# Kernel optimization log

Hardware: AMD Instinct MI355X
Metric: run time of the kernel (lower is better)

The kernel has to match this reference:

```python
import jax, jax.numpy as jnp
import numpy as np

P_SIZE = 5
NUM_HEAD = 8
GN_EPS = 1e-5


def _conv1x1(w, x, b=None):
    # w: (out_c, in_c), x: (n, in_c, h, w)
    y = jnp.einsum('oc,nchw->nohw', w, x)
    if b is not None:
        y = y + b[None, :, None, None]
    return y


def _leaky_relu(x, slope=0.2):
    return jnp.where(x >= 0, x, slope * x)


def _bilinear_sample_zeros(feat, vx, vy):
    # feat: (c, H, W); vx, vy: (p2, H, W) pixel coords (align_corners=True,
    # padding_mode='zeros'). Returns (c, p2, H, W).
    c, H, W = feat.shape
    x0 = jnp.floor(vx)
    y0 = jnp.floor(vy)
    x1 = x0 + 1.0
    y1 = y0 + 1.0
    wx1 = vx - x0
    wy1 = vy - y0
    wx0 = 1.0 - wx1
    wy0 = 1.0 - wy1

    def corner(xi, yi, wgt):
        valid = (xi >= 0) & (xi <= W - 1) & (yi >= 0) & (yi <= H - 1)
        xc = jnp.clip(xi, 0, W - 1).astype(jnp.int32)
        yc = jnp.clip(yi, 0, H - 1).astype(jnp.int32)
        g = feat[:, yc, xc]  # (c, p2, H, W)
        return g * (wgt * valid)[None]

    return (corner(x0, y0, wx0 * wy0) + corner(x1, y0, wx1 * wy0)
            + corner(x0, y1, wx0 * wy1) + corner(x1, y1, wx1 * wy1))


def _deform_coords(deform_field, h, w, p_size):
    # deform_field: (n, 2, h, w) -> vx, vy: (n, p2, h, w) pixel coords.
    pad = (p_size - 1) // 2
    gy, gx = jnp.meshgrid(jnp.arange(h, dtype=deform_field.dtype),
                          jnp.arange(w, dtype=deform_field.dtype), indexing='ij')
    shift = jnp.arange(p_size, dtype=deform_field.dtype) - pad
    sy, sx = jnp.meshgrid(shift, shift, indexing='ij')
    sy = sy.reshape(-1, 1, 1)
    sx = sx.reshape(-1, 1, 1)
    vx = gx[None] + sx + deform_field[:, None, 0]  # (n, p2, h, w)
    vy = gy[None] + sy + deform_field[:, None, 1]
    return vx, vy


def _transformer_forward(query, key, value, deform_field,
                         w_q, w_k, w_v, w_fc,
                         mlp_w1, mlp_b1, mlp_w2, mlp_b2, gn_w, gn_b):
    p2 = P_SIZE * P_SIZE
    q = _conv1x1(w_q, query)
    k = _conv1x1(w_k, key)
    v = _conv1x1(w_v, value)
    n, c, h, w = q.shape
    d_k = c // NUM_HEAD

    vx, vy = _deform_coords(deform_field, h, w, P_SIZE)
    sample = jax.vmap(_bilinear_sample_zeros)  # over batch
    k_s = sample(k, vx, vy)  # (n, c, p2, h, w)
    v_s = sample(v, vx, vy)

    qh = q.reshape(n, NUM_HEAD, d_k, h, w)
    kh = k_s.reshape(n, NUM_HEAD, d_k, p2, h, w)
    vh = v_s.reshape(n, NUM_HEAD, d_k, p2, h, w)

    scale = 1.0 / jnp.sqrt(jnp.asarray(d_k, q.dtype))
    scores = jnp.einsum('nedyx,nedpyx->neyxp', qh * scale, kh)
    attn = jax.nn.softmax(scores, axis=-1)
    out = jnp.einsum('neyxp,nedpyx->nedyx', attn, vh).reshape(n, c, h, w)
    out = _conv1x1(w_fc, out)

    hid = _leaky_relu(_conv1x1(mlp_w1, out, mlp_b1))
    out = out + _conv1x1(mlp_w2, hid, mlp_b2)

    # GroupNorm(1, c): normalize over (c, h, w) per sample
    mean = jnp.mean(out, axis=(1, 2, 3), keepdims=True)
    var = jnp.var(out, axis=(1, 2, 3), keepdims=True)
    out = (out - mean) * jax.lax.rsqrt(var + GN_EPS)
    out = out * gn_w[None, :, None, None] + gn_b[None, :, None, None]
    return out


def setup_inputs() -> dict:
    key = jax.random.key(0)
    ks = jax.random.split(key, 12)
    n, C, H, W = 1, 128, 128, 128
    hidden = C * 2
    s = 1.0 / np.sqrt(C)
    return {
        'query': jax.random.normal(ks[0], (n, C, H, W), jnp.float32),
        'key': jax.random.normal(ks[1], (n, C, H, W), jnp.float32),
        'value': jax.random.normal(ks[2], (n, C, H, W), jnp.float32),
        'deform_field': jax.random.normal(ks[3], (n, 2, H, W), jnp.float32) * 2.0,
        'w_q': jax.random.normal(ks[4], (C, C), jnp.float32) * s,
        'w_k': jax.random.normal(ks[5], (C, C), jnp.float32) * s,
        'w_v': jax.random.normal(ks[6], (C, C), jnp.float32) * s,
        'w_fc': jax.random.normal(ks[7], (C, C), jnp.float32) * s,
        'mlp_w1': jax.random.normal(ks[8], (hidden, C), jnp.float32) * s,
        'mlp_b1': jnp.zeros((hidden,), jnp.float32),
        'mlp_w2': jax.random.normal(ks[9], (C, hidden), jnp.float32) * (1.0 / np.sqrt(hidden)),
        'mlp_b2': jnp.zeros((C,), jnp.float32),
        'gn_w': jnp.ones((C,), jnp.float32),
        'gn_b': jnp.zeros((C,), jnp.float32),
    }


def reference(query, key, value, deform_field, w_q, w_k, w_v, w_fc,
              mlp_w1, mlp_b1, mlp_w2, mlp_b2, gn_w, gn_b):
    return _transformer_forward(query, key, value, deform_field,
                                w_q, w_k, w_v, w_fc,
                                mlp_w1, mlp_b1, mlp_w2, mlp_b2, gn_w, gn_b)
```

## Files before the change

kernel.cpp:

```cpp
#include <hip/hip_runtime.h>
#include <hip/hip_bf16.h>

#define HW 16384
#define W 128
#define C 128
#define HID 256

typedef __attribute__((ext_vector_type(8))) short short8v;
typedef __attribute__((ext_vector_type(4))) float f32x4;

__device__ __forceinline__ unsigned short f2bf(float f) {
    union { float f; unsigned u; } x; x.f = f;
    unsigned r = x.u + 0x7FFF + ((x.u >> 16) & 1);
    return (unsigned short)(r >> 16);
}
__device__ __forceinline__ float bf2f(unsigned short b) {
    union { unsigned u; float f; } x; x.u = ((unsigned)b) << 16;
    return x.f;
}

__device__ __forceinline__ void stage_load(const unsigned short* __restrict__ src,
                                           short8v* r, int t) {
    #pragma unroll
    for (int c = 0; c < 8; ++c)
        r[c] = *(const short8v*)(src + (size_t)(c * 256 + t) * 8);
}
template<int RSH>
__device__ __forceinline__ void stage_write(const short8v* r, unsigned short* lds, int t) {
    #pragma unroll
    for (int c = 0; c < 8; ++c) {
        int gi = c * 256 + t;
        int row = gi >> RSH, colg = gi & ((1 << RSH) - 1);
        *(short8v*)(lds + (size_t)(((row << RSH) + (colg ^ (row & 7))) << 3)) = r[c];
    }
}
template<int RSH>
__device__ __forceinline__ void stage32(const unsigned short* __restrict__ src,
                                        unsigned short* lds, int t) {
    #pragma unroll
    for (int c = 0; c < 8; ++c) {
        int gi = c * 256 + t;
        int row = gi >> RSH, colg = gi & ((1 << RSH) - 1);
        short8v v = *(const short8v*)(src + (size_t)gi * 8);
        *(short8v*)(lds + (size_t)(((row << RSH) + (colg ^ (row & 7))) << 3)) = v;
    }
}

__global__ void prep_weights(const float* __restrict__ wq, const float* __restrict__ wk,
                             const float* __restrict__ wv, const float* __restrict__ wfc,
                             const float* __restrict__ w1, const float* __restrict__ w2,
                             unsigned short* __restrict__ wb) {
    int i = blockIdx.x * 256 + threadIdx.x;
    float v;
    if (i < 16384)       v = wq[i];
    else if (i < 32768)  v = wk[i - 16384];
    else if (i < 49152)  v = wv[i - 32768];
    else if (i < 65536)  v = wfc[i - 49152];
    else if (i < 98304)  v = w1[i - 65536];
    else                 v = w2[i - 98304];
    wb[i] = f2bf(v);
}

__global__ __launch_bounds__(256, 2)
void qkv_mfma(const float* __restrict__ q_in, const float* __restrict__ k_in,
              const float* __restrict__ v_in, const unsigned short* __restrict__ wb,
              unsigned short* __restrict__ q_t, unsigned short* __restrict__ kv_t) {
    __shared__ unsigned short lx[3][32 * 128];
    __shared__ unsigned short wbuf[16384];
    const int t = threadIdx.x;
    const int p0 = blockIdx.x * 32;
    const int lane = t & 63, row16 = lane & 15, g = lane >> 4;
    const int w = t >> 6, nh = w & 1, mh = w >> 1;
    const int ploc = nh * 16 + row16;
    const int pix = p0 + ploc;
    const int swz = (ploc & 7) << 3;

    stage32<4>(wb, wbuf, t);

    const float* ins[3] = {q_in, k_in, v_in};
    #pragma unroll
    for (int m = 0; m < 3; ++m) {
        #pragma unroll
        for (int it = 0; it < 16; ++it) {
            int e = t + 256 * it;
            int p = e & 31, c = e >> 5;
            lx[m][p * 128 + (c ^ ((p & 7) << 3))] = f2bf(ins[m][c * HW + p0 + p]);
        }
    }

    #pragma unroll 1
    for (int m = 0; m < 3; ++m) {
        if (m > 0) {
            __syncthreads();
            stage32<4>(wb + m * 16384, wbuf, t);
        }
        __syncthreads();

        f32x4 acc[4] = {};
        #pragma unroll
        for (int kk = 0; kk < 4; ++kk) {
            short8v b = *(const short8v*)&lx[m][ploc * 128 + ((kk * 32 + g * 8) ^ swz)];
            #pragma unroll
            for (int f = 0; f < 4; ++f) {
                int row = mh * 64 + f * 16 + row16;
                short8v a = *(const short8v*)&wbuf[(row << 7) + (((kk * 4 + g) ^ (row & 7)) << 3)];
                acc[f] = __builtin_amdgcn_mfma_f32_16x16x32_bf16(a, b, acc[f], 0, 0, 0);
            }
        }
        #pragma unroll
        for (int f = 0; f < 4; ++f) {
            int o = mh * 64 + f * 16 + g * 4;
            ushort4 st;
            st.x = f2bf(acc[f][0]); st.y = f2bf(acc[f][1]);
            st.z = f2bf(acc[f][2]); st.w = f2bf(acc[f][3]);
            if (m == 0)      *(ushort4*)&q_t[(size_t)pix * 128 + o] = st;
            else if (m == 1) *(ushort4*)&kv_t[(size_t)pix * 256 + o] = st;
            else             *(ushort4*)&kv_t[(size_t)pix * 256 + 128 + o] = st;
        }
    }
}

__global__ __launch_bounds__(256, 2)
void attn_kernel(const unsigned short* __restrict__ q_t, const unsigned short* __restrict__ kv_t,
                 const float* __restrict__ deform, unsigned short* __restrict__ ao_t) {
    const int t = threadIdx.x;
    const int pi = t >> 4;
    const int g = t & 15;
    const char* kvb = (const char*)kv_t;
    const int go = g * 16;

    const int jj = blockIdx.x;
    const int y = jj >> 3;
    const int x = ((jj & 7) << 4) + pi;
    const int pix = y * W + x;

    const float dx = deform[pix];
    const float dy = deform[HW + pix];
    const float fdx = floorf(dx), fdy = floorf(dy);
    const float fx = dx - fdx, fy = dy - fdy;
    const float wx0 = 1.f - fx, wx1 = fx, wy0 = 1.f - fy, wy1 = fy;
    const int x0 = x - 2 + (int)fdx;
    const int y0 = y - 2 + (int)fdy;

    int   coff[6], roff[6];
    float colv[6], rowv[6];
    #pragma unroll
    for (int j = 0; j < 6; ++j) {
        int xc = x0 + j, yc = y0 + j;
        colv[j] = ((unsigned)xc <= 127u) ? 1.f : 0.f;
        rowv[j] = ((unsigned)yc <= 127u) ? 1.f : 0.f;
        coff[j] = (min(max(xc, 0), 127) << 9) + go;
        roff[j] = min(max(yc, 0), 127) << 16;
    }

    float q[8];
    {
        short8v qv = *(const short8v*)(q_t + (size_t)pix * C + g * 8);
        #pragma unroll
        for (int e = 0; e < 8; ++e) q[e] = bf2f((unsigned short)qv[e]) * 0.25f;
    }

    float d[36];
    #pragma unroll
    for (int jy = 0; jy < 6; ++jy) {
        #pragma unroll
        for (int jx = 0; jx < 6; ++jx) {
            short8v k = *(const short8v*)(kvb + (roff[jy] + coff[jx]));
            float dd = 0.f;
            #pragma unroll
            for (int e = 0; e < 8; ++e) dd += q[e] * bf2f((unsigned short)k[e]);
            d[jy * 6 + jx] = dd * (rowv[jy] * colv[jx]);
        }
    }

    float s[25];
    #pragma unroll
    for (int iy = 0; iy < 5; ++iy) {
        #pragma unroll
        for (int ix = 0; ix < 5; ++ix) {
            float sp = wy0 * (wx0 * d[iy * 6 + ix]       + wx1 * d[iy * 6 + ix + 1])
                     + wy1 * (wx0 * d[(iy + 1) * 6 + ix] + wx1 * d[(iy + 1) * 6 + ix + 1]);
            sp += __shfl_xor(sp, 1);
            s[iy * 5 + ix] = sp;
        }
    }

    float m = s[0];
    #pragma unroll
    for (int p = 1; p < 25; ++p) m = fmaxf(m, s[p]);
    float sum = 0.f;
    #pragma unroll
    for (int p = 0; p < 25; ++p) {
        float e = __expf(s[p] - m);
        s[p] = e;
        sum += e;
    }
    const float inv = 1.f / sum;

    float b[36];
    #pragma unroll
    for (int jy = 0; jy < 6; ++jy) {
        #pragma unroll
        for (int jx = 0; jx < 6; ++jx) {
            float acc = 0.f;
            if (jy < 5  && jx < 5)  acc += wy0 * wx0 * s[jy * 5 + jx];
            if (jy < 5  && jx >= 1) acc += wy0 * wx1 * s[jy * 5 + jx - 1];
            if (jy >= 1 && jx < 5)  acc += wy1 * wx0 * s[(jy - 1) * 5 + jx];
            if (jy >= 1 && jx >= 1) acc += wy1 * wx1 * s[(jy - 1) * 5 + jx - 1];
            b[jy * 6 + jx] = acc * (rowv[jy] * colv[jx]);
        }
    }

    float oc[8] = {0.f, 0.f, 0.f, 0.f, 0.f, 0.f, 0.f, 0.f};
    #pragma unroll
    for (int jy = 0; jy < 6; ++jy) {
        #pragma unroll
        for (int jx = 0; jx < 6; ++jx) {
            short8v v = *(const short8v*)(kvb + (roff[jy] + coff[jx]) + 256);
            float bw = b[jy * 6 + jx];
            #pragma unroll
            for (int e = 0; e < 8; ++e) oc[e] += bw * bf2f((unsigned short)v[e]);
        }
    }

    short8v ob;
    #pragma unroll
    for (int e = 0; e < 8; ++e) ob[e] = (short)f2bf(oc[e] * inv);
    *(short8v*)(ao_t + (size_t)pix * C + g * 8) = ob;
}

__global__ __launch_bounds__(256, 2)
void mlp_mfma(const unsigned short* __restrict__ ao_t, const unsigned short* __restrict__ wb,
              const float* __restrict__ b1, const float* __restrict__ b2,
              float* __restrict__ out2, float2* __restrict__ partials) {
    __shared__ unsigned short wbuf[16384];
    __shared__ unsigned short l1[64 * 128];
    __shared__ unsigned short lh[64 * 256];
    __shared__ float rs[8];
    const int t = threadIdx.x;
    const int p0 = blockIdx.x * 64;
    const int lane = t & 63, row16 = lane & 15, g = lane >> 4;
    const int w = t >> 6, nh = w & 1, mh = w >> 1;
    const unsigned short* wfc_b = wb + 49152;
    const unsigned short* w1_b  = wb + 65536;
    const unsigned short* w2_b  = wb + 98304;

    short8v r[8];
    stage_load(wfc_b, r, t);
    short8v bf[2][4];
    #pragma unroll
    for (int st = 0; st < 2; ++st) {
        int pix = p0 + st * 32 + nh * 16 + row16;
        #pragma unroll
        for (int kk = 0; kk < 4; ++kk)
            bf[st][kk] = *(const short8v*)&ao_t[(size_t)pix * 128 + kk * 32 + g * 8];
    }
    stage_write<4>(r, wbuf, t);
    __syncthreads();

    stage_load(w1_b, r, t);
    #pragma unroll
    for (int st = 0; st < 2; ++st) {
        const int ploc = st * 32 + nh * 16 + row16;
        const int swz = (ploc & 7) << 3;
        f32x4 acc[4] = {};
        #pragma unroll
        for (int kk = 0; kk < 4; ++kk) {
            #pragma unroll
            for (int f = 0; f < 4; ++f) {
                int row = mh * 64 + f * 16 + row16;
                short8v a = *(const short8v*)&wbuf[(row << 7) + (((kk * 4 + g) ^ (row & 7)) << 3)];
                acc[f] = __builtin_amdgcn_mfma_f32_16x16x32_bf16(a, bf[st][kk], acc[f], 0, 0, 0);
            }
        }
        #pragma unroll
        for (int f = 0; f < 4; ++f)
            #pragma unroll
            for (int e = 0; e < 4; ++e) {
                int o = mh * 64 + f * 16 + g * 4 + e;
                l1[ploc * 128 + (o ^ swz)] = f2bf(acc[f][e]);
            }
    }
    __syncthreads();
    stage_write<4>(r, wbuf, t);
    __syncthreads();

    #pragma unroll
    for (int s = 0; s < 2; ++s) {
        if (s == 0) stage_load(w1_b + 16384, r, t);
        else        stage_load(w2_b, r, t);
        #pragma unroll
        for (int st = 0; st < 2; ++st) {
            const int ploc = st * 32 + nh * 16 + row16;
            const int swz = (ploc & 7) << 3;
            f32x4 acc[4] = {};
            #pragma unroll
            for (int kk = 0; kk < 4; ++kk) {
                short8v b = *(const short8v*)&l1[ploc * 128 + ((kk * 32 + g * 8) ^ swz)];
                #pragma unroll
                for (int f = 0; f < 4; ++f) {
                    int row = mh * 64 + f * 16 + row16;
                    short8v a = *(const short8v*)&wbuf[(row << 7) + (((kk * 4 + g) ^ (row & 7)) << 3)];
                    acc[f] = __builtin_amdgcn_mfma_f32_16x16x32_bf16(a, b, acc[f], 0, 0, 0);
                }
            }
            #pragma unroll
            for (int f = 0; f < 4; ++f) {
                int h = s * 128 + mh * 64 + f * 16 + g * 4;
                float4 bb = *(const float4*)&b1[h];
                float hv[4] = {acc[f][0] + bb.x, acc[f][1] + bb.y,
                               acc[f][2] + bb.z, acc[f][3] + bb.w};
                #pragma unroll
                for (int e = 0; e < 4; ++e) {
                    float v = (hv[e] >= 0.f) ? hv[e] : 0.2f * hv[e];
                    lh[ploc * 256 + ((h + e) ^ swz)] = f2bf(v);
                }
            }
        }
        __syncthreads();
        if (s == 0) stage_write<4>(r, wbuf, t);
        else        stage_write<5>(r, wbuf, t);
        __syncthreads();
    }

    float lsum = 0.f, lsq = 0.f;
    #pragma unroll
    for (int s = 0; s < 2; ++s) {
        if (s == 0) stage_load(w2_b + 16384, r, t);
        #pragma unroll
        for (int st = 0; st < 2; ++st) {
            const int ploc = st * 32 + nh * 16 + row16;
            const int swz = (ploc & 7) << 3;
            const int pix = p0 + ploc;
            f32x4 acc[2] = {};
            #pragma unroll
            for (int kk = 0; kk < 8; ++kk) {
                short8v b = *(const short8v*)&lh[ploc * 256 + ((kk * 32 + g * 8) ^ swz)];
                #pragma unroll
                for (int f = 0; f < 2; ++f) {
                    int row = mh * 32 + f * 16 + row16;
                    short8v a = *(const short8v*)&wbuf[(row << 8) + (((kk * 4 + g) ^ (row & 7)) << 3)];
                    acc[f] = __builtin_amdgcn_mfma_f32_16x16x32_bf16(a, b, acc[f], 0, 0, 0);
                }
            }
            #pragma unroll
            for (int f = 0; f < 2; ++f) {
                int ob = s * 64 + mh * 32 + f * 16 + g * 4;
                float4 b2v = *(const float4*)&b2[ob];
                ushort4 res = *(const ushort4*)&l1[ploc * 128 + (ob ^ swz)];
                float bv[4] = {b2v.x, b2v.y, b2v.z, b2v.w};
                unsigned short rr[4] = {res.x, res.y, res.z, res.w};
                #pragma unroll
                for (int e = 0; e < 4; ++e) {
                    float v = acc[f][e] + bf2f(rr[e]) + bv[e];
                    out2[(size_t)(ob + e) * HW + pix] = v;
                    lsum += v;
                    lsq += v * v;
                }
            }
        }
        if (s == 0) {
            __syncthreads();
            stage_write<5>(r, wbuf, t);
            __syncthreads();
        }
    }

    #pragma unroll
    for (int s = 1; s < 64; s <<= 1) {
        lsum += __shfl_xor(lsum, s);
        lsq  += __shfl_xor(lsq, s);
    }
    if (lane == 0) { rs[w] = lsum; rs[4 + w] = lsq; }
    __syncthreads();
    if (t == 0)
        partials[blockIdx.x] = make_float2(rs[0] + rs[1] + rs[2] + rs[3],
                                           rs[4] + rs[5] + rs[6] + rs[7]);
}

__global__ void norm_kernel(float* __restrict__ out2, const float2* __restrict__ partials,
                            const float* __restrict__ gn_w, const float* __restrict__ gn_b) {
    __shared__ float rs[8];
    __shared__ float stat[2];
    const int t = threadIdx.x;

    float2 p = partials[t];
    float a = p.x, bb = p.y;
    #pragma unroll
    for (int s = 1; s < 64; s <<= 1) {
        a  += __shfl_xor(a, s);
        bb += __shfl_xor(bb, s);
    }
    if ((t & 63) == 0) { rs[t >> 6] = a; rs[4 + (t >> 6)] = bb; }
    __syncthreads();
    if (t == 0) {
        const float invN = 1.f / 2097152.f;
        float mean = (rs[0] + rs[1] + rs[2] + rs[3]) * invN;
        float var = (rs[4] + rs[5] + rs[6] + rs[7]) * invN - mean * mean;
        stat[0] = mean;
        stat[1] = rsqrtf(var + 1e-5f);
    }
    __syncthreads();

    const float mean = stat[0], rstd = stat[1];
    const int gid = blockIdx.x * 256 + t;
    int base = gid * 4;
    int o = base >> 14;
    float g = gn_w[o] * rstd;
    float b = gn_b[o];
    float4 v = *(const float4*)(out2 + base);
    float4 r;
    r.x = (v.x - mean) * g + b;
    r.y = (v.y - mean) * g + b;
    r.z = (v.z - mean) * g + b;
    r.w = (v.w - mean) * g + b;
    *(float4*)(out2 + base) = r;
}

extern "C" void kernel_launch(void* const* d_in, const int* in_sizes, int n_in,
                              void* d_out, int out_size, void* d_ws, size_t ws_size,
                              hipStream_t stream) {
    const float* query  = (const float*)d_in[0];
    const float* key    = (const float*)d_in[1];
    const float* value  = (const float*)d_in[2];
    const float* deform = (const float*)d_in[3];
    const float* w_q    = (const float*)d_in[4];
    const float* w_k    = (const float*)d_in[5];
    const float* w_v    = (const float*)d_in[6];
    const float* w_fc   = (const float*)d_in[7];
    const float* mlp_w1 = (const float*)d_in[8];
    const float* mlp_b1 = (const float*)d_in[9];
    const float* mlp_w2 = (const float*)d_in[10];
    const float* mlp_b2 = (const float*)d_in[11];
    const float* gn_w   = (const float*)d_in[12];
    const float* gn_b   = (const float*)d_in[13];

    float* out = (float*)d_out;
    char* wsb  = (char*)d_ws;

    unsigned short* q_t  = (unsigned short*)wsb;
    unsigned short* kv_t = (unsigned short*)(wsb + ((size_t)4 << 20));
    unsigned short* ao_t = (unsigned short*)(wsb + ((size_t)12 << 20));
    unsigned short* wb   = (unsigned short*)(wsb + ((size_t)16 << 20));
    float2* partials = (float2*)(wsb + ((size_t)17 << 20));

    prep_weights<<<512, 256, 0, stream>>>(w_q, w_k, w_v, w_fc, mlp_w1, mlp_w2, wb);
    qkv_mfma<<<512, 256, 0, stream>>>(query, key, value, wb, q_t, kv_t);
    attn_kernel<<<1024, 256, 0, stream>>>(q_t, kv_t, deform, ao_t);
    mlp_mfma<<<256, 256, 0, stream>>>(ao_t, wb, mlp_b1, mlp_b2, out, partials);
    norm_kernel<<<2048, 256, 0, stream>>>(out, partials, gn_w, gn_b);
}
```

Baseline: 52.93 us.

## Fold weight conversion into qkv kernel and halve MLP pixel tile

Removes the separate prep_weights launch. The qkv kernel now reads fp32 q/k/v weights directly and converts them to bf16 while staging into LDS, and its blocks also convert the fc/MLP weights into the bf16 workspace for the later kernel. The MLP kernel processes 32 pixels per block instead of 64 and launches 512 blocks, so norm_kernel now sums 512 partials. This saves a launch and adds parallelism in the MLP stage, at the cost of each qkv block redundantly converting fp32 weights and each MLP block restaging weights for fewer pixels.

```diff
diff --git a/kernel.cpp b/kernel.cpp
--- a/kernel.cpp
+++ b/kernel.cpp
@@ -35,35 +35,31 @@
     }
 }
 template<int RSH>
-__device__ __forceinline__ void stage32(const unsigned short* __restrict__ src,
-                                        unsigned short* lds, int t) {
+__device__ __forceinline__ void stage32f(const float* __restrict__ src,
+                                         unsigned short* lds, int t) {
     #pragma unroll
     for (int c = 0; c < 8; ++c) {
         int gi = c * 256 + t;
         int row = gi >> RSH, colg = gi & ((1 << RSH) - 1);
-        short8v v = *(const short8v*)(src + (size_t)gi * 8);
+        float4 a = *(const float4*)(src + (size_t)gi * 8);
+        float4 b = *(const float4*)(src + (size_t)gi * 8 + 4);
+        short8v v;
+        v[0] = (short)f2bf(a.x); v[1] = (short)f2bf(a.y);
+        v[2] = (short)f2bf(a.z); v[3] = (short)f2bf(a.w);
+        v[4] = (short)f2bf(b.x); v[5] = (short)f2bf(b.y);
+        v[6] = (short)f2bf(b.z); v[7] = (short)f2bf(b.w);
         *(short8v*)(lds + (size_t)(((row << RSH) + (colg ^ (row & 7))) << 3)) = v;
     }
-}
-
-__global__ void prep_weights(const float* __restrict__ wq, const float* __restrict__ wk,
-                             const float* __restrict__ wv, const float* __restrict__ wfc,
-                             const float* __restrict__ w1, const float* __restrict__ w2,
-                             unsigned short* __restrict__ wb) {
-    int i = blockIdx.x * 256 + threadIdx.x;
-    float v;
-    if (i < 16384)       v = wq[i];
-    else if (i < 32768)  v = wk[i - 16384];
-    else if (i < 49152)  v = wv[i - 32768];
-    else if (i < 65536)  v = wfc[i - 49152];
-    else if (i < 98304)  v = w1[i - 65536];
-    else                 v = w2[i - 98304];
-    wb[i] = f2bf(v);
 }
 
 __global__ __launch_bounds__(256, 2)
 void qkv_mfma(const float* __restrict__ q_in, const float* __restrict__ k_in,
-              const float* __restrict__ v_in, const unsigned short* __restrict__ wb,
+              const float* __restrict__ v_in,
+              const float* __restrict__ w_q, const float* __restrict__ w_k,
+              const float* __restrict__ w_v,
+              const float* __restrict__ wfc, const float* __restrict__ w1,
+              const float* __restrict__ w2,
+              unsigned short* __restrict__ wb,
               unsigned short* __restrict__ q_t, unsigned short* __restrict__ kv_t) {
     __shared__ unsigned short lx[3][32 * 128];
     __shared__ unsigned short wbuf[16384];
@@ -75,7 +71,13 @@
     const int pix = p0 + ploc;
     const int swz = (ploc & 7) << 3;
 
-    stage32<4>(wb, wbuf, t);
+    stage32f<4>(w_q, wbuf, t);
+
+    if (t < 192) {
+        int i = blockIdx.x * 192 + t;
+        float v = (i < 16384) ? wfc[i] : (i < 49152) ? w1[i - 16384] : w2[i - 49152];
+        wb[i] = f2bf(v);
+    }
 
     const float* ins[3] = {q_in, k_in, v_in};
     #pragma unroll
@@ -88,11 +90,12 @@
         }
     }
 
+    const float* ws[3] = {w_q, w_k, w_v};
     #pragma unroll 1
     for (int m = 0; m < 3; ++m) {
         if (m > 0) {
             __syncthreads();
-            stage32<4>(wb + m * 16384, wbuf, t);
+            stage32f<4>(ws[m], wbuf, t);
         }
         __syncthreads();
 
@@ -234,35 +237,31 @@
               const float* __restrict__ b1, const float* __restrict__ b2,
               float* __restrict__ out2, float2* __restrict__ partials) {
     __shared__ unsigned short wbuf[16384];
-    __shared__ unsigned short l1[64 * 128];
-    __shared__ unsigned short lh[64 * 256];
+    __shared__ unsigned short l1[32 * 128];
+    __shared__ unsigned short lh[32 * 256];
     __shared__ float rs[8];
     const int t = threadIdx.x;
-    const int p0 = blockIdx.x * 64;
+    const int p0 = blockIdx.x * 32;
     const int lane = t & 63, row16 = lane & 15, g = lane >> 4;
     const int w = t >> 6, nh = w & 1, mh = w >> 1;
-    const unsigned short* wfc_b = wb + 49152;
-    const unsigned short* w1_b  = wb + 65536;
-    const unsigned short* w2_b  = wb + 98304;
+    const int ploc = nh * 16 + row16;
+    const int pix = p0 + ploc;
+    const int swz = (ploc & 7) << 3;
+    const unsigned short* wfc_b = wb;
+    const unsigned short* w1_b  = wb + 16384;
+    const unsigned short* w2_b  = wb + 49152;
 
     short8v r[8];
     stage_load(wfc_b, r, t);
-    short8v bf[2][4];
-    #pragma unroll
-    for (int st = 0; st < 2; ++st) {
-        int pix = p0 + st * 32 + nh * 16 + row16;
-        #pragma unroll
-        for (int kk = 0; kk < 4; ++kk)
-            bf[st][kk] = *(const short8v*)&ao_t[(size_t)pix * 128 + kk * 32 + g * 8];
-    }
+    short8v bf[4];
+    #pragma unroll
+    for (int kk = 0; kk < 4; ++kk)
+        bf[kk] = *(const short8v*)&ao_t[(size_t)pix * 128 + kk * 32 + g * 8];
     stage_write<4>(r, wbuf, t);
     __syncthreads();
 
     stage_load(w1_b, r, t);
-    #pragma unroll
-    for (int st = 0; st < 2; ++st) {
-        const int ploc = st * 32 + nh * 16 + row16;
-        const int swz = (ploc & 7) << 3;
+    {
         f32x4 acc[4] = {};
         #pragma unroll
         for (int kk = 0; kk < 4; ++kk) {
@@ -270,7 +269,7 @@
             for (int f = 0; f < 4; ++f) {
                 int row = mh * 64 + f * 16 + row16;
                 short8v a = *(const short8v*)&wbuf[(row << 7) + (((kk * 4 + g) ^ (row & 7)) << 3)];
-                acc[f] = __builtin_amdgcn_mfma_f32_16x16x32_bf16(a, bf[st][kk], acc[f], 0, 0, 0);
+                acc[f] = __builtin_amdgcn_mfma_f32_16x16x32_bf16(a, bf[kk], acc[f], 0, 0, 0);
             }
         }
         #pragma unroll
@@ -289,32 +288,27 @@
     for (int s = 0; s < 2; ++s) {
         if (s == 0) stage_load(w1_b + 16384, r, t);
         else        stage_load(w2_b, r, t);
-        #pragma unroll
-        for (int st = 0; st < 2; ++st) {
-            const int ploc = st * 32 + nh * 16 + row16;
-            const int swz = (ploc & 7) << 3;
-            f32x4 acc[4] = {};
-            #pragma unroll
-            for (int kk = 0; kk < 4; ++kk) {
-                short8v b = *(const short8v*)&l1[ploc * 128 + ((kk * 32 + g * 8) ^ swz)];
-                #pragma unroll
-                for (int f = 0; f < 4; ++f) {
-                    int row = mh * 64 + f * 16 + row16;
-                    short8v a = *(const short8v*)&wbuf[(row << 7) + (((kk * 4 + g) ^ (row & 7)) << 3)];
-                    acc[f] = __builtin_amdgcn_mfma_f32_16x16x32_bf16(a, b, acc[f], 0, 0, 0);
-                }
-            }
+        f32x4 acc[4] = {};
+        #pragma unroll
+        for (int kk = 0; kk < 4; ++kk) {
+            short8v b = *(const short8v*)&l1[ploc * 128 + ((kk * 32 + g * 8) ^ swz)];
             #pragma unroll
             for (int f = 0; f < 4; ++f) {
-                int h = s * 128 + mh * 64 + f * 16 + g * 4;
-                float4 bb = *(const float4*)&b1[h];
-                float hv[4] = {acc[f][0] + bb.x, acc[f][1] + bb.y,
-                               acc[f][2] + bb.z, acc[f][3] + bb.w};
-                #pragma unroll
-                for (int e = 0; e < 4; ++e) {
-                    float v = (hv[e] >= 0.f) ? hv[e] : 0.2f * hv[e];
-                    lh[ploc * 256 + ((h + e) ^ swz)] = f2bf(v);
-                }
+                int row = mh * 64 + f * 16 + row16;
+                short8v a = *(const short8v*)&wbuf[(row << 7) + (((kk * 4 + g) ^ (row & 7)) << 3)];
+                acc[f] = __builtin_amdgcn_mfma_f32_16x16x32_bf16(a, b, acc[f], 0, 0, 0);
+            }
+        }
+        #pragma unroll
+        for (int f = 0; f < 4; ++f) {
+            int h = s * 128 + mh * 64 + f * 16 + g * 4;
+            float4 bb = *(const float4*)&b1[h];
+            float hv[4] = {acc[f][0] + bb.x, acc[f][1] + bb.y,
+                           acc[f][2] + bb.z, acc[f][3] + bb.w};
+            #pragma unroll
+            for (int e = 0; e < 4; ++e) {
+                float v = (hv[e] >= 0.f) ? hv[e] : 0.2f * hv[e];
+                lh[ploc * 256 + ((h + e) ^ swz)] = f2bf(v);
             }
         }
         __syncthreads();
@@ -327,36 +321,30 @@
     #pragma unroll
     for (int s = 0; s < 2; ++s) {
         if (s == 0) stage_load(w2_b + 16384, r, t);
-        #pragma unroll
-        for (int st = 0; st < 2; ++st) {
-            const int ploc = st * 32 + nh * 16 + row16;
-            const int swz = (ploc & 7) << 3;
-            const int pix = p0 + ploc;
-            f32x4 acc[2] = {};
-            #pragma unroll
-            for (int kk = 0; kk < 8; ++kk) {
-                short8v b = *(const short8v*)&lh[ploc * 256 + ((kk * 32 + g * 8) ^ swz)];
-                #pragma unroll
-                for (int f = 0; f < 2; ++f) {
-                    int row = mh * 32 + f * 16 + row16;
-                    short8v a = *(const short8v*)&wbuf[(row << 8) + (((kk * 4 + g) ^ (row & 7)) << 3)];
-                    acc[f] = __builtin_amdgcn_mfma_f32_16x16x32_bf16(a, b, acc[f], 0, 0, 0);
-                }
-            }
+        f32x4 acc[2] = {};
+        #pragma unroll
+        for (int kk = 0; kk < 8; ++kk) {
+            short8v b = *(const short8v*)&lh[ploc * 256 + ((kk * 32 + g * 8) ^ swz)];
             #pragma unroll
             for (int f = 0; f < 2; ++f) {
-                int ob = s * 64 + mh * 32 + f * 16 + g * 4;
-                float4 b2v = *(const float4*)&b2[ob];
-                ushort4 res = *(const ushort4*)&l1[ploc * 128 + (ob ^ swz)];
-                float bv[4] = {b2v.x, b2v.y, b2v.z, b2v.w};
-                unsigned short rr[4] = {res.x, res.y, res.z, res.w};
-                #pragma unroll
-                for (int e = 0; e < 4; ++e) {
-                    float v = acc[f][e] + bf2f(rr[e]) + bv[e];
-                    out2[(size_t)(ob + e) * HW + pix] = v;
-                    lsum += v;
-                    lsq += v * v;
-                }
+                int row = mh * 32 + f * 16 + row16;
+                short8v a = *(const short8v*)&wbuf[(row << 8) + (((kk * 4 + g) ^ (row & 7)) << 3)];
+                acc[f] = __builtin_amdgcn_mfma_f32_16x16x32_bf16(a, b, acc[f], 0, 0, 0);
+            }
+        }
+        #pragma unroll
+        for (int f = 0; f < 2; ++f) {
+            int ob = s * 64 + mh * 32 + f * 16 + g * 4;
+            float4 b2v = *(const float4*)&b2[ob];
+            ushort4 res = *(const ushort4*)&l1[ploc * 128 + (ob ^ swz)];
+            float bv[4] = {b2v.x, b2v.y, b2v.z, b2v.w};
+            unsigned short rr[4] = {res.x, res.y, res.z, res.w};
+            #pragma unroll
+            for (int e = 0; e < 4; ++e) {
+                float v = acc[f][e] + bf2f(rr[e]) + bv[e];
+                out2[(size_t)(ob + e) * HW + pix] = v;
+                lsum += v;
+                lsq += v * v;
             }
         }
         if (s == 0) {
@@ -384,8 +372,9 @@
     __shared__ float stat[2];
     const int t = threadIdx.x;
 
-    float2 p = partials[t];
-    float a = p.x, bb = p.y;
+    float2 p0 = partials[t];
+    float2 p1 = partials[t + 256];
+    float a = p0.x + p1.x, bb = p0.y + p1.y;
     #pragma unroll
     for (int s = 1; s < 64; s <<= 1) {
         a  += __shfl_xor(a, s);
@@ -444,9 +433,9 @@
     unsigned short* wb   = (unsigned short*)(wsb + ((size_t)16 << 20));
     float2* partials = (float2*)(wsb + ((size_t)17 << 20));
 
-    prep_weights<<<512, 256, 0, stream>>>(w_q, w_k, w_v, w_fc, mlp_w1, mlp_w2, wb);
-    qkv_mfma<<<512, 256, 0, stream>>>(query, key, value, wb, q_t, kv_t);
+    qkv_mfma<<<512, 256, 0, stream>>>(query, key, value, w_q, w_k, w_v,
+                                      w_fc, mlp_w1, mlp_w2, wb, q_t, kv_t);
     attn_kernel<<<1024, 256, 0, stream>>>(q_t, kv_t, deform, ao_t);
-    mlp_mfma<<<256, 256, 0, stream>>>(ao_t, wb, mlp_b1, mlp_b2, out, partials);
+    mlp_mfma<<<512, 256, 0, stream>>>(ao_t, wb, mlp_b1, mlp_b2, out, partials);
     norm_kernel<<<2048, 256, 0, stream>>>(out, partials, gn_w, gn_b);
 }
```

Result: faster. 49.72 us (-6.1%).
